# Performance work log

Measured on AMD Instinct MI355X. Metric: run time of the kernel, lower is better.

The kernel has to match this reference:

```python
import jax, jax.numpy as jnp
import numpy as np

N, C, D, K = 4096, 512, 64, 10  # samples, clusters (c_max), feature_dim, num_classes
KAPPA_N = 10.0


def setup_inputs() -> dict:
    key = jax.random.key(0)
    k1, k2, k3, k4, k5, k6 = jax.random.split(key, 6)
    data = jax.random.normal(k1, (N, D), dtype=jnp.float32)
    labels = jax.random.randint(k2, (N,), 0, K)
    # cluster support counts n >= kappa_n (mature clusters)
    n = jax.random.uniform(k3, (C,), dtype=jnp.float32) * 90.0 + KAPPA_N
    mu = jax.random.normal(k4, (C, D), dtype=jnp.float32) * 2.0
    # S is the scatter matrix; covariance Sigma = S / n must be SPD, so
    # build S = n * (0.1 * A A^T + 0.5 I)
    A = jax.random.normal(k5, (C, D, D), dtype=jnp.float32)
    AAT = jnp.einsum('cij,ckj->cik', A, A) / D
    S = n[:, None, None] * (0.1 * AAT + 0.5 * jnp.eye(D, dtype=jnp.float32))
    # one-hot class label per cluster
    cls = jax.random.randint(k6, (C,), 0, K)
    cluster_labels = jax.nn.one_hot(cls, K, dtype=jnp.int32)
    return {"data": data, "labels": labels, "n": n, "mu": mu, "S": S,
            "cluster_labels": cluster_labels}


def reference(data, labels, n, mu, S, cluster_labels):
    # Inference path of eGAUSSp.forward: for each sample z,
    #   Gamma_j = exp(-0.5 * (z - mu_j)^T (S_j / n_j)^{-1} (z - mu_j))   (all c clusters)
    #   scores  = defuzzify = sum_j Gamma_j * onehot(label_j) / sum_j Gamma_j
    # Vectorized over the batch (no cross-sample dependence in eval mode).
    eps = jnp.asarray(1e-6, data.dtype)
    Sigma = S / n[:, None, None] + eps * jnp.eye(S.shape[-1], dtype=data.dtype)  # [C,D,D]
    Sinv = jnp.linalg.inv(Sigma)                                                  # [C,D,D]
    diff = data[:, None, :] - mu[None, :, :]          # [N,C,D]
    tmp = jnp.einsum('ncd,cde->nce', diff, Sinv)      # [N,C,D]
    d2 = jnp.einsum('nce,nce->nc', tmp, diff)         # [N,C] squared Mahalanobis
    Gamma = jnp.exp(-0.5 * d2)                        # [N,C] activations
    lab_f = cluster_labels.astype(data.dtype)         # [C,K]
    scores = (Gamma @ lab_f) / (jnp.sum(Gamma, axis=1, keepdims=True) + 1e-12)  # [N,K]
    pred = jnp.argmax(scores, axis=1)
    clusters = jnp.argmax(Gamma, axis=1)
    return scores, pred, clusters
```

## Files before the change

### kernel.cpp

```cpp
#include <hip/hip_runtime.h>
#include <hip/hip_bf16.h>
#include <math.h>

#define NS 4096
#define NC 512
#define ND 64
#define NK 10
#define NPAIR 2080
#define KP 2176
#define BOFF 2080
#define KOFF 2144
#define KSPLIT 4
#define KT_PER (KP / 32 / KSPLIT)
#define ZB 1024
#define QB 2048

typedef __attribute__((ext_vector_type(8))) short short8;
typedef __attribute__((ext_vector_type(4))) float floatx4;

__device__ inline unsigned short f2b(float x) {
    __hip_bfloat16 h = __float2bfloat16(x);
    return __builtin_bit_cast(unsigned short, h);
}
__device__ inline float b2f(unsigned short u) {
    __hip_bfloat16 h = __builtin_bit_cast(__hip_bfloat16, u);
    return __bfloat162float(h);
}

__device__ inline float rlane(float v, int k) {
    return __builtin_bit_cast(float, __builtin_amdgcn_readlane(__builtin_bit_cast(int, v), k));
}

__device__ inline void gl16(const void* g, void* l) {
    __builtin_amdgcn_global_load_lds(
        (const __attribute__((address_space(1))) unsigned int*)g,
        (__attribute__((address_space(3))) unsigned int*)l, 16, 0, 0);
}

__device__ inline uchar2 ed_decode(int p) {
    if (p < NPAIR) {
        const float s = sqrtf((float)(16641 - 8 * p));
        int e = (int)((129.0f - s) * 0.5f);
        int off = e * 64 - (e * (e - 1)) / 2;
        const int offn = off + (64 - e);
        if (p >= offn) { off = offn; ++e; }
        else if (p < off) { off -= (65 - e); --e; }
        return make_uchar2((unsigned char)e, (unsigned char)(e + (p - off)));
    } else if (p < KOFF) return make_uchar2((unsigned char)(p - BOFF), 64);
    else if (p == KOFF)  return make_uchar2(64, 64);
    return make_uchar2(65, 65);
}

__global__ __launch_bounds__(256, 4) void prep_kernel(
    const float* __restrict__ data, const float* __restrict__ S,
    const float* __restrict__ n, const float* __restrict__ mu,
    const int* __restrict__ clab,
    unsigned short* __restrict__ Qh, unsigned short* __restrict__ Ql,
    unsigned short* __restrict__ Bph, unsigned short* __restrict__ Bpl,
    float* __restrict__ d2, float* __restrict__ labf)
{
    __shared__ float AcolS[ND * (ND + 1)];
    __shared__ float cbuf[ND];
    __shared__ float rowbuf[2][ND];
    __shared__ float kksS[1];
    __shared__ float zq[2][66];

    if (blockIdx.x >= NC + ZB) {
        const int qb = blockIdx.x - (NC + ZB);
        const int half = threadIdx.x >> 7;
        const int i = threadIdx.x & 127;
        const int row = qb * 2 + half;
        if (i < 64) zq[half][i] = data[(size_t)row * ND + i];
        else if (i == 64) { zq[half][64] = 1.0f; zq[half][65] = 0.0f; }
        __syncthreads();
        const float* __restrict__ zr = zq[half];
        unsigned short* __restrict__ qh = Qh + (size_t)row * KP;
        unsigned short* __restrict__ ql = Ql + (size_t)row * KP;
        #pragma unroll
        for (int t = 0; t < 17; ++t) {
            const int p = t * 128 + i;
            const uchar2 ed = ed_decode(p);
            const float v = zr[ed.x] * zr[ed.y];
            const unsigned short h = f2b(v);
            const unsigned short l = f2b(v - b2f(h));
            qh[p] = h;
            ql[p] = l;
        }
        return;
    }

    if (blockIdx.x >= NC) {
        const size_t base = (size_t)(blockIdx.x - NC) * 2048 + threadIdx.x * 8;
        *(float4*)&d2[base]     = make_float4(0.f, 0.f, 0.f, 0.f);
        *(float4*)&d2[base + 4] = make_float4(0.f, 0.f, 0.f, 0.f);
        return;
    }

    const int c = blockIdx.x;
    const int tid = threadIdx.x;
    const int j = tid & 63;
    const int w = tid >> 6;
    const int rbase = w * 16;

    const float inv_nc = 1.0f / n[c];
    const float* __restrict__ Sc = S + (size_t)c * ND * ND + j;

    float4 B0, B1, B2, B3;
#define LOADR(u) {                                                   \
    const float x0 = Sc[(rbase + 4*(u) + 0) * ND] * inv_nc;          \
    const float x1 = Sc[(rbase + 4*(u) + 1) * ND] * inv_nc;          \
    const float x2 = Sc[(rbase + 4*(u) + 2) * ND] * inv_nc;          \
    const float x3 = Sc[(rbase + 4*(u) + 3) * ND] * inv_nc;          \
    B##u.x = (rbase + 4*(u) + 0 == j) ? x0 + 1e-6f : x0;             \
    B##u.y = (rbase + 4*(u) + 1 == j) ? x1 + 1e-6f : x1;             \
    B##u.z = (rbase + 4*(u) + 2 == j) ? x2 + 1e-6f : x2;             \
    B##u.w = (rbase + 4*(u) + 3 == j) ? x3 + 1e-6f : x3; }
    LOADR(0) LOADR(1) LOADR(2) LOADR(3)
#undef LOADR

#define UPD4(u, K) {                                                  \
    const float c0 = rlane(B##u.x, K);                                \
    const float c1 = rlane(B##u.y, K);                                \
    const float c2 = rlane(B##u.z, K);                                \
    const float c3 = rlane(B##u.w, K);                                \
    B##u.x = (om && (4*(u)+0 == ((K)&15))) ? rowk : B##u.x * am - c0 * rowk; \
    B##u.y = (om && (4*(u)+1 == ((K)&15))) ? rowk : B##u.y * am - c1 * rowk; \
    B##u.z = (om && (4*(u)+2 == ((K)&15))) ? rowk : B##u.z * am - c2 * rowk; \
    B##u.w = (om && (4*(u)+3 == ((K)&15))) ? rowk : B##u.w * am - c3 * rowk; \
}
#define STEPC(TL, C, K) {                                             \
    if (w == ((K) >> 4)) {                                            \
        const float rp = B##TL.C;          \
        const float pv = rlane(rp, K);             \
        const float ip = 1.0f / pv;                                   \
        rowbuf[(K) & 1][j] = (j == (K)) ? ip : rp * ip;               \
    }                                                                 \
    __syncthreads();                                                  \
    const float rowk = rowbuf[(K) & 1][j];                            \
    const float am = (j == (K)) ? 0.0f : 1.0f;                        \
    const bool om = (w == ((K) >> 4));                                \
    UPD4(0, K) UPD4(1, K) UPD4(2, K) UPD4(3, K)                       \
}
#define STEP4(T, TL) STEPC(TL, x, 4*(T)+0) STEPC(TL, y, 4*(T)+1) \
                     STEPC(TL, z, 4*(T)+2) STEPC(TL, w, 4*(T)+3)
#define FOR16P(M) M(0,0) M(1,1) M(2,2) M(3,3) M(4,0) M(5,1) M(6,2) M(7,3) \
                  M(8,0) M(9,1) M(10,2) M(11,3) M(12,0) M(13,1) M(14,2) M(15,3)
    FOR16P(STEP4)
#undef FOR16P
#undef STEP4
#undef STEPC
#undef UPD4

#define MIR(u) *(float4*)&AcolS[j * (ND + 1) + rbase + 4*(u)] = B##u;
    MIR(0) MIR(1) MIR(2) MIR(3)
#undef MIR
    __syncthreads();

    if (w == 0) {
        const float* __restrict__ muc = mu + (size_t)c * ND;
        float y = 0.f;
        #pragma unroll
        for (int t = 0; t < 16; ++t) {
            const float4 v = *(const float4*)&AcolS[j * (ND + 1) + 4 * t];
            y += v.x * muc[4*t]     + v.y * muc[4*t + 1]
               + v.z * muc[4*t + 2] + v.w * muc[4*t + 3];
        }
        cbuf[j] = -2.0f * y;
        float kk = muc[j] * y;
        #pragma unroll
        for (int off = 32; off > 0; off >>= 1) kk += __shfl_down(kk, off);
        if (j == 0) {
            kksS[0] = kk;
            int lab = 0;
            for (int q = 0; q < NK; ++q) if (clab[c * NK + q] != 0) lab = q;
            labf[c] = (float)lab;
        }
    }
    __syncthreads();
    const float kks = kksS[0];

    unsigned short* __restrict__ ph = Bph + (size_t)c * KP;
    unsigned short* __restrict__ pl = Bpl + (size_t)c * KP;
    #pragma unroll
    for (int i = 0; i < 9; ++i) {
        const int t = w + 4 * i;
        if (t < KP / 64) {
            const int p = t * 64 + j;
            float val;
            if (p < NPAIR) {
                const uchar2 ed = ed_decode(p);
                val = (ed.x == ed.y) ? AcolS[ed.x * (ND + 1) + ed.x]
                    : (AcolS[ed.y * (ND + 1) + ed.x] + AcolS[ed.x * (ND + 1) + ed.y]);
            } else if (p < KOFF) val = cbuf[p - BOFF];
            else if (p == KOFF)  val = kks;
            else                 val = 0.f;
            const unsigned short h = f2b(val);
            const unsigned short l = f2b(val - b2f(h));
            ph[p] = h;
            pl[p] = l;
        }
    }
}

__global__ __launch_bounds__(256, 2) void gemm_kernel(
    const unsigned short* __restrict__ Qh, const unsigned short* __restrict__ Ql,
    const unsigned short* __restrict__ Bph, const unsigned short* __restrict__ Bpl,
    float* __restrict__ d2)
{
    __shared__ unsigned short AhS[2][64 * 32], AlS[2][64 * 32];
    __shared__ unsigned short BhS[2][256 * 32], BlS[2][256 * 32];

    const int tid  = threadIdx.x;
    const int lane = tid & 63, w = tid >> 6;
    const int quad = lane >> 4, rlo = lane & 15;

    const int lid = blockIdx.x + 64 * blockIdx.y + 128 * blockIdx.z;
    const int nyz = lid & 7;
    const int m0 = (lid >> 3) * 64;
    const int n0 = (nyz & 1) * 256;
    const int koff0 = (nyz >> 1) * KT_PER * 32;

    const int srow = tid >> 2;
    const int sswz = (tid & 3) ^ ((srow >> 2) & 3);
    const unsigned short* aGh = Qh + (size_t)(m0 + srow) * KP + koff0 + sswz * 8;
    const unsigned short* aGl = Ql + (size_t)(m0 + srow) * KP + koff0 + sswz * 8;
    const unsigned short* bGh[4];
    const unsigned short* bGl[4];
    #pragma unroll
    for (int rd = 0; rd < 4; ++rd) {
        const size_t off = (size_t)(n0 + rd * 64 + srow) * KP + koff0 + sswz * 8;
        bGh[rd] = Bph + off;
        bGl[rd] = Bpl + off;
    }
    const int swz8 = (quad ^ ((rlo >> 2) & 3)) * 8;

    floatx4 acc[4][4] = {};

#define STAGE(b, t) {                                                 \
        const int _ko = (t) * 32;                                     \
        gl16(aGh + _ko, &AhS[b][tid * 8]);                            \
        gl16(aGl + _ko, &AlS[b][tid * 8]);                            \
        _Pragma("unroll")                                             \
        for (int rd = 0; rd < 4; ++rd) {                              \
            gl16(bGh[rd] + _ko, &BhS[b][(rd * 256 + tid) * 8]);       \
            gl16(bGl[rd] + _ko, &BlS[b][(rd * 256 + tid) * 8]);       \
        } }

    STAGE(0, 0)
    STAGE(1, 1)
    asm volatile("s_waitcnt vmcnt(10)" ::: "memory");
    __builtin_amdgcn_s_barrier();

    for (int kt = 0; kt < KT_PER; ++kt) {
        const int cur = kt & 1;

        short8 ah[4], al[4], bh[4], bl[4];
        #pragma unroll
        for (int i = 0; i < 4; ++i) {
            ah[i] = *(const short8*)&AhS[cur][(i * 16 + rlo) * 32 + swz8];
            al[i] = *(const short8*)&AlS[cur][(i * 16 + rlo) * 32 + swz8];
        }
        #pragma unroll
        for (int j2 = 0; j2 < 4; ++j2) {
            const int r = w * 64 + j2 * 16 + rlo;
            bh[j2] = *(const short8*)&BhS[cur][r * 32 + swz8];
            bl[j2] = *(const short8*)&BlS[cur][r * 32 + swz8];
        }
        asm volatile("s_waitcnt lgkmcnt(0)" ::: "memory");
        __builtin_amdgcn_sched_barrier(0);
        __builtin_amdgcn_s_barrier();

        if (kt < KT_PER - 2) STAGE(cur, kt + 2)

        __builtin_amdgcn_s_setprio(1);
        #pragma unroll
        for (int i = 0; i < 4; ++i)
            #pragma unroll
            for (int j2 = 0; j2 < 4; ++j2) {
                acc[i][j2] = __builtin_amdgcn_mfma_f32_16x16x32_bf16(al[i], bh[j2], acc[i][j2], 0, 0, 0);
                acc[i][j2] = __builtin_amdgcn_mfma_f32_16x16x32_bf16(ah[i], bl[j2], acc[i][j2], 0, 0, 0);
                acc[i][j2] = __builtin_amdgcn_mfma_f32_16x16x32_bf16(ah[i], bh[j2], acc[i][j2], 0, 0, 0);
            }
        __builtin_amdgcn_s_setprio(0);

        if (kt < KT_PER - 2) {
            asm volatile("s_waitcnt vmcnt(10)" ::: "memory");
        } else {
            asm volatile("s_waitcnt vmcnt(0)" ::: "memory");
        }
        __builtin_amdgcn_s_barrier();
    }
#undef STAGE

    #pragma unroll
    for (int i = 0; i < 4; ++i)
        #pragma unroll
        for (int j2 = 0; j2 < 4; ++j2) {
            const int m = m0 + i * 16 + quad * 4;
            const int nn = n0 + w * 64 + j2 * 16 + rlo;
            #pragma unroll
            for (int r = 0; r < 4; ++r)
                atomicAdd(&d2[(size_t)(m + r) * NC + nn], acc[i][j2][r]);
        }
}

__global__ __launch_bounds__(256) void score_kernel(
    const float* __restrict__ d2, const float* __restrict__ labf,
    float* __restrict__ out)
{
    const int s = blockIdx.x * 4 + (threadIdx.x >> 6);
    const int l = threadIdx.x & 63;

    float numer[NK];
    #pragma unroll
    for (int q = 0; q < NK; ++q) numer[q] = 0.f;
    float denom = 0.f, gmax = -1.f;
    int gidx = 0;

    #pragma unroll
    for (int i = 0; i < NC / 256; ++i) {
        const int c0 = i * 256 + l * 4;
        const float4 v = *(const float4*)&d2[(size_t)s * NC + c0];
        #pragma unroll
        for (int r = 0; r < 4; ++r) {
            const int c = c0 + r;
            const float G = __expf(-0.5f * ((const float*)&v)[r]);
            denom += G;
            const int lab = (int)labf[c];
            #pragma unroll
            for (int q = 0; q < NK; ++q) numer[q] += (q == lab) ? G : 0.f;
            if (G > gmax) { gmax = G; gidx = c; }
        }
    }

    #pragma unroll
    for (int off = 32; off > 0; off >>= 1) {
        const float og = __shfl_down(gmax, off);
        const int   oi = __shfl_down(gidx, off);
        if (og > gmax || (og == gmax && oi < gidx)) { gmax = og; gidx = oi; }
        denom += __shfl_down(denom, off);
        #pragma unroll
        for (int q = 0; q < NK; ++q) numer[q] += __shfl_down(numer[q], off);
    }

    if (l == 0) {
        const float inv = 1.0f / (denom + 1e-12f);
        float best = -1.f; int pk = 0;
        #pragma unroll
        for (int q = 0; q < NK; ++q) {
            const float sc = numer[q] * inv;
            out[(size_t)s * NK + q] = sc;
            if (sc > best) { best = sc; pk = q; }
        }
        out[(size_t)NS * NK + s]      = (float)pk;
        out[(size_t)NS * NK + NS + s] = (float)gidx;
    }
}

extern "C" void kernel_launch(void* const* d_in, const int* in_sizes, int n_in,
                              void* d_out, int out_size, void* d_ws, size_t ws_size,
                              hipStream_t stream)
{
    const float* data = (const float*)d_in[0];
    const float* n    = (const float*)d_in[2];
    const float* mu   = (const float*)d_in[3];
    const float* S    = (const float*)d_in[4];
    const int*   clab = (const int*)d_in[5];

    char* w = (char*)d_ws;
    unsigned short* Qh  = (unsigned short*)(w);
    unsigned short* Ql  = (unsigned short*)(w + 17825792);
    unsigned short* Bph = (unsigned short*)(w + 35651584);
    unsigned short* Bpl = (unsigned short*)(w + 37879808);
    float* d2   = (float*)(w + 40108032);
    float* labf = (float*)(w + 48496640);

    hipLaunchKernelGGL(prep_kernel,  dim3(NC + ZB + QB), dim3(256), 0, stream,
                       data, S, n, mu, clab, Qh, Ql, Bph, Bpl, d2, labf);
    hipLaunchKernelGGL(gemm_kernel,  dim3(NS / 64, NC / 256, KSPLIT), dim3(256), 0, stream,
                       Qh, Ql, Bph, Bpl, d2);
    hipLaunchKernelGGL(score_kernel, dim3(NS / 4), dim3(256), 0, stream,
                       d2, labf, (float*)d_out);
}
```

Baseline: 149.2 us.

## Fuse prep, GEMM and scoring into one cooperative kernel with grid syncs

Replaces the three separate launches (prep, split-K GEMM, score) with a single cooperative kernel of 512 blocks. Each block zeroes part of d2, builds Q rows for 8 samples and inverts one cluster covariance, then passes a grid sync, runs one GEMM tile, passes another grid sync and scores 8 samples. This removes launch gaps and kernel boundaries, at the cost of grid-wide barriers. It also needs every block resident at once under the shared-memory union and launch bounds, and the prep phase runs on fewer blocks than before.

```diff
diff --git a/kernel.cpp b/kernel.cpp
--- a/kernel.cpp
+++ b/kernel.cpp
@@ -1,6 +1,9 @@
 #include <hip/hip_runtime.h>
+#include <hip/hip_cooperative_groups.h>
 #include <hip/hip_bf16.h>
 #include <math.h>
+
+namespace cg = cooperative_groups;
 
 #define NS 4096
 #define NC 512
@@ -12,8 +15,6 @@
 #define KOFF 2144
 #define KSPLIT 4
 #define KT_PER (KP / 32 / KSPLIT)
-#define ZB 1024
-#define QB 2048
 
 typedef __attribute__((ext_vector_type(8))) short short8;
 typedef __attribute__((ext_vector_type(4))) float floatx4;
@@ -51,61 +52,81 @@
     return make_uchar2(65, 65);
 }
 
-__global__ __launch_bounds__(256, 4) void prep_kernel(
+union SmemU {
+    struct {
+        unsigned short AhS[2][64 * 32], AlS[2][64 * 32];
+        unsigned short BhS[2][256 * 32], BlS[2][256 * 32];
+    } g;
+    struct {
+        float AcolS[ND * (ND + 1)];
+        float cbuf[ND];
+        float rowbuf[2][ND];
+        float kks[1];
+        float zq[8][66];
+    } p;
+};
+
+__global__ __launch_bounds__(256, 2) void mega_kernel(
     const float* __restrict__ data, const float* __restrict__ S,
     const float* __restrict__ n, const float* __restrict__ mu,
     const int* __restrict__ clab,
     unsigned short* __restrict__ Qh, unsigned short* __restrict__ Ql,
     unsigned short* __restrict__ Bph, unsigned short* __restrict__ Bpl,
-    float* __restrict__ d2, float* __restrict__ labf)
+    float* __restrict__ d2, float* __restrict__ labf, float* __restrict__ out)
 {
-    __shared__ float AcolS[ND * (ND + 1)];
-    __shared__ float cbuf[ND];
-    __shared__ float rowbuf[2][ND];
-    __shared__ float kksS[1];
-    __shared__ float zq[2][66];
-
-    if (blockIdx.x >= NC + ZB) {
-        const int qb = blockIdx.x - (NC + ZB);
-        const int half = threadIdx.x >> 7;
-        const int i = threadIdx.x & 127;
-        const int row = qb * 2 + half;
-        if (i < 64) zq[half][i] = data[(size_t)row * ND + i];
-        else if (i == 64) { zq[half][64] = 1.0f; zq[half][65] = 0.0f; }
+    __shared__ SmemU sm;
+    cg::grid_group grid = cg::this_grid();
+
+    const int tid  = threadIdx.x;
+    const int lane = tid & 63, w = tid >> 6;
+    const int quad = lane >> 4, rlo = lane & 15;
+    const int blk  = blockIdx.x;
+
+    {
+        const size_t base = (size_t)blk * 4096 + tid * 16;
+        *(float4*)&d2[base]      = make_float4(0.f, 0.f, 0.f, 0.f);
+        *(float4*)&d2[base + 4]  = make_float4(0.f, 0.f, 0.f, 0.f);
+        *(float4*)&d2[base + 8]  = make_float4(0.f, 0.f, 0.f, 0.f);
+        *(float4*)&d2[base + 12] = make_float4(0.f, 0.f, 0.f, 0.f);
+    }
+
+    {
+        const int r8 = tid >> 5;
+        const int cc = (tid & 31) * 2;
+        sm.p.zq[r8][cc]     = data[(size_t)(blk * 8 + r8) * ND + cc];
+        sm.p.zq[r8][cc + 1] = data[(size_t)(blk * 8 + r8) * ND + cc + 1];
+        if ((tid & 31) == 0) { sm.p.zq[r8][64] = 1.0f; sm.p.zq[r8][65] = 0.0f; }
         __syncthreads();
-        const float* __restrict__ zr = zq[half];
-        unsigned short* __restrict__ qh = Qh + (size_t)row * KP;
-        unsigned short* __restrict__ ql = Ql + (size_t)row * KP;
-        #pragma unroll
-        for (int t = 0; t < 17; ++t) {
-            const int p = t * 128 + i;
-            const uchar2 ed = ed_decode(p);
-            const float v = zr[ed.x] * zr[ed.y];
-            const unsigned short h = f2b(v);
-            const unsigned short l = f2b(v - b2f(h));
-            qh[p] = h;
-            ql[p] = l;
-        }
-        return;
-    }
-
-    if (blockIdx.x >= NC) {
-        const size_t base = (size_t)(blockIdx.x - NC) * 2048 + threadIdx.x * 8;
-        *(float4*)&d2[base]     = make_float4(0.f, 0.f, 0.f, 0.f);
-        *(float4*)&d2[base + 4] = make_float4(0.f, 0.f, 0.f, 0.f);
-        return;
-    }
-
-    const int c = blockIdx.x;
-    const int tid = threadIdx.x;
-    const int j = tid & 63;
-    const int w = tid >> 6;
-    const int rbase = w * 16;
-
-    const float inv_nc = 1.0f / n[c];
-    const float* __restrict__ Sc = S + (size_t)c * ND * ND + j;
-
-    float4 B0, B1, B2, B3;
+        const int half = tid >> 7;
+        const int i = tid & 127;
+        #pragma unroll
+        for (int rr = 0; rr < 4; ++rr) {
+            const int row = blk * 8 + rr * 2 + half;
+            const float* __restrict__ zr = sm.p.zq[rr * 2 + half];
+            unsigned short* __restrict__ qh = Qh + (size_t)row * KP;
+            unsigned short* __restrict__ ql = Ql + (size_t)row * KP;
+            #pragma unroll
+            for (int t = 0; t < 17; ++t) {
+                const int p = t * 128 + i;
+                const uchar2 ed = ed_decode(p);
+                const float v = zr[ed.x] * zr[ed.y];
+                const unsigned short h = f2b(v);
+                const unsigned short l = f2b(v - b2f(h));
+                qh[p] = h;
+                ql[p] = l;
+            }
+        }
+    }
+
+    {
+        const int c = blk;
+        const int j = lane;
+        const int rbase = w * 16;
+
+        const float inv_nc = 1.0f / n[c];
+        const float* __restrict__ Sc = S + (size_t)c * ND * ND + j;
+
+        float4 B0, B1, B2, B3;
 #define LOADR(u) {                                                   \
     const float x0 = Sc[(rbase + 4*(u) + 0) * ND] * inv_nc;          \
     const float x1 = Sc[(rbase + 4*(u) + 1) * ND] * inv_nc;          \
@@ -115,7 +136,7 @@
     B##u.y = (rbase + 4*(u) + 1 == j) ? x1 + 1e-6f : x1;             \
     B##u.z = (rbase + 4*(u) + 2 == j) ? x2 + 1e-6f : x2;             \
     B##u.w = (rbase + 4*(u) + 3 == j) ? x3 + 1e-6f : x3; }
-    LOADR(0) LOADR(1) LOADR(2) LOADR(3)
+        LOADR(0) LOADR(1) LOADR(2) LOADR(3)
 #undef LOADR
 
 #define UPD4(u, K) {                                                  \
@@ -130,13 +151,13 @@
 }
 #define STEPC(TL, C, K) {                                             \
     if (w == ((K) >> 4)) {                                            \
-        const float rp = B##TL.C;          \
-        const float pv = rlane(rp, K);             \
+        const float rp = B##TL.C;                                     \
+        const float pv = rlane(rp, K);                                \
         const float ip = 1.0f / pv;                                   \
-        rowbuf[(K) & 1][j] = (j == (K)) ? ip : rp * ip;               \
+        sm.p.rowbuf[(K) & 1][j] = (j == (K)) ? ip : rp * ip;          \
     }                                                                 \
     __syncthreads();                                                  \
-    const float rowk = rowbuf[(K) & 1][j];                            \
+    const float rowk = sm.p.rowbuf[(K) & 1][j];                       \
     const float am = (j == (K)) ? 0.0f : 1.0f;                        \
     const bool om = (w == ((K) >> 4));                                \
     UPD4(0, K) UPD4(1, K) UPD4(2, K) UPD4(3, K)                       \
@@ -145,215 +166,209 @@
                      STEPC(TL, z, 4*(T)+2) STEPC(TL, w, 4*(T)+3)
 #define FOR16P(M) M(0,0) M(1,1) M(2,2) M(3,3) M(4,0) M(5,1) M(6,2) M(7,3) \
                   M(8,0) M(9,1) M(10,2) M(11,3) M(12,0) M(13,1) M(14,2) M(15,3)
-    FOR16P(STEP4)
+        FOR16P(STEP4)
 #undef FOR16P
 #undef STEP4
 #undef STEPC
 #undef UPD4
 
-#define MIR(u) *(float4*)&AcolS[j * (ND + 1) + rbase + 4*(u)] = B##u;
-    MIR(0) MIR(1) MIR(2) MIR(3)
+#define MIR(u) *(float4*)&sm.p.AcolS[j * (ND + 1) + rbase + 4*(u)] = B##u;
+        MIR(0) MIR(1) MIR(2) MIR(3)
 #undef MIR
-    __syncthreads();
-
-    if (w == 0) {
-        const float* __restrict__ muc = mu + (size_t)c * ND;
-        float y = 0.f;
-        #pragma unroll
-        for (int t = 0; t < 16; ++t) {
-            const float4 v = *(const float4*)&AcolS[j * (ND + 1) + 4 * t];
-            y += v.x * muc[4*t]     + v.y * muc[4*t + 1]
-               + v.z * muc[4*t + 2] + v.w * muc[4*t + 3];
-        }
-        cbuf[j] = -2.0f * y;
-        float kk = muc[j] * y;
-        #pragma unroll
-        for (int off = 32; off > 0; off >>= 1) kk += __shfl_down(kk, off);
-        if (j == 0) {
-            kksS[0] = kk;
-            int lab = 0;
-            for (int q = 0; q < NK; ++q) if (clab[c * NK + q] != 0) lab = q;
-            labf[c] = (float)lab;
-        }
-    }
-    __syncthreads();
-    const float kks = kksS[0];
-
-    unsigned short* __restrict__ ph = Bph + (size_t)c * KP;
-    unsigned short* __restrict__ pl = Bpl + (size_t)c * KP;
-    #pragma unroll
-    for (int i = 0; i < 9; ++i) {
-        const int t = w + 4 * i;
-        if (t < KP / 64) {
-            const int p = t * 64 + j;
-            float val;
-            if (p < NPAIR) {
-                const uchar2 ed = ed_decode(p);
-                val = (ed.x == ed.y) ? AcolS[ed.x * (ND + 1) + ed.x]
-                    : (AcolS[ed.y * (ND + 1) + ed.x] + AcolS[ed.x * (ND + 1) + ed.y]);
-            } else if (p < KOFF) val = cbuf[p - BOFF];
-            else if (p == KOFF)  val = kks;
-            else                 val = 0.f;
-            const unsigned short h = f2b(val);
-            const unsigned short l = f2b(val - b2f(h));
-            ph[p] = h;
-            pl[p] = l;
-        }
-    }
-}
-
-__global__ __launch_bounds__(256, 2) void gemm_kernel(
-    const unsigned short* __restrict__ Qh, const unsigned short* __restrict__ Ql,
-    const unsigned short* __restrict__ Bph, const unsigned short* __restrict__ Bpl,
-    float* __restrict__ d2)
-{
-    __shared__ unsigned short AhS[2][64 * 32], AlS[2][64 * 32];
-    __shared__ unsigned short BhS[2][256 * 32], BlS[2][256 * 32];
-
-    const int tid  = threadIdx.x;
-    const int lane = tid & 63, w = tid >> 6;
-    const int quad = lane >> 4, rlo = lane & 15;
-
-    const int lid = blockIdx.x + 64 * blockIdx.y + 128 * blockIdx.z;
-    const int nyz = lid & 7;
-    const int m0 = (lid >> 3) * 64;
-    const int n0 = (nyz & 1) * 256;
-    const int koff0 = (nyz >> 1) * KT_PER * 32;
-
-    const int srow = tid >> 2;
-    const int sswz = (tid & 3) ^ ((srow >> 2) & 3);
-    const unsigned short* aGh = Qh + (size_t)(m0 + srow) * KP + koff0 + sswz * 8;
-    const unsigned short* aGl = Ql + (size_t)(m0 + srow) * KP + koff0 + sswz * 8;
-    const unsigned short* bGh[4];
-    const unsigned short* bGl[4];
-    #pragma unroll
-    for (int rd = 0; rd < 4; ++rd) {
-        const size_t off = (size_t)(n0 + rd * 64 + srow) * KP + koff0 + sswz * 8;
-        bGh[rd] = Bph + off;
-        bGl[rd] = Bpl + off;
-    }
-    const int swz8 = (quad ^ ((rlo >> 2) & 3)) * 8;
-
-    floatx4 acc[4][4] = {};
+        __syncthreads();
+
+        if (w == 0) {
+            const float* __restrict__ muc = mu + (size_t)c * ND;
+            float y = 0.f;
+            #pragma unroll
+            for (int t = 0; t < 16; ++t) {
+                const float4 v = *(const float4*)&sm.p.AcolS[j * (ND + 1) + 4 * t];
+                y += v.x * muc[4*t]     + v.y * muc[4*t + 1]
+                   + v.z * muc[4*t + 2] + v.w * muc[4*t + 3];
+            }
+            sm.p.cbuf[j] = -2.0f * y;
+            float kk = muc[j] * y;
+            #pragma unroll
+            for (int off = 32; off > 0; off >>= 1) kk += __shfl_down(kk, off);
+            if (j == 0) {
+                sm.p.kks[0] = kk;
+                int lab = 0;
+                for (int q = 0; q < NK; ++q) if (clab[c * NK + q] != 0) lab = q;
+                labf[c] = (float)lab;
+            }
+        }
+        __syncthreads();
+        const float kks = sm.p.kks[0];
+
+        unsigned short* __restrict__ ph = Bph + (size_t)c * KP;
+        unsigned short* __restrict__ pl = Bpl + (size_t)c * KP;
+        #pragma unroll
+        for (int i2 = 0; i2 < 9; ++i2) {
+            const int t = w + 4 * i2;
+            if (t < KP / 64) {
+                const int p = t * 64 + j;
+                float val;
+                if (p < NPAIR) {
+                    const uchar2 ed = ed_decode(p);
+                    val = (ed.x == ed.y) ? sm.p.AcolS[ed.x * (ND + 1) + ed.x]
+                        : (sm.p.AcolS[ed.y * (ND + 1) + ed.x] + sm.p.AcolS[ed.x * (ND + 1) + ed.y]);
+                } else if (p < KOFF) val = sm.p.cbuf[p - BOFF];
+                else if (p == KOFF)  val = kks;
+                else                 val = 0.f;
+                const unsigned short h = f2b(val);
+                const unsigned short l = f2b(val - b2f(h));
+                ph[p] = h;
+                pl[p] = l;
+            }
+        }
+    }
+
+    grid.sync();
+
+    {
+        const int lid = blk;
+        const int nyz = lid & 7;
+        const int m0 = (lid >> 3) * 64;
+        const int n0 = (nyz & 1) * 256;
+        const int koff0 = (nyz >> 1) * KT_PER * 32;
+
+        const int srow = tid >> 2;
+        const int sswz = (tid & 3) ^ ((srow >> 2) & 3);
+        const unsigned short* aGh = Qh + (size_t)(m0 + srow) * KP + koff0 + sswz * 8;
+        const unsigned short* aGl = Ql + (size_t)(m0 + srow) * KP + koff0 + sswz * 8;
+        const unsigned short* bGh[4];
+        const unsigned short* bGl[4];
+        #pragma unroll
+        for (int rd = 0; rd < 4; ++rd) {
+            const size_t off = (size_t)(n0 + rd * 64 + srow) * KP + koff0 + sswz * 8;
+            bGh[rd] = Bph + off;
+            bGl[rd] = Bpl + off;
+        }
+        const int swz8 = (quad ^ ((rlo >> 2) & 3)) * 8;
+
+        floatx4 acc[4][4] = {};
 
 #define STAGE(b, t) {                                                 \
         const int _ko = (t) * 32;                                     \
-        gl16(aGh + _ko, &AhS[b][tid * 8]);                            \
-        gl16(aGl + _ko, &AlS[b][tid * 8]);                            \
+        gl16(aGh + _ko, &sm.g.AhS[b][tid * 8]);                       \
+        gl16(aGl + _ko, &sm.g.AlS[b][tid * 8]);                       \
         _Pragma("unroll")                                             \
         for (int rd = 0; rd < 4; ++rd) {                              \
-            gl16(bGh[rd] + _ko, &BhS[b][(rd * 256 + tid) * 8]);       \
-            gl16(bGl[rd] + _ko, &BlS[b][(rd * 256 + tid) * 8]);       \
+            gl16(bGh[rd] + _ko, &sm.g.BhS[b][(rd * 256 + tid) * 8]);  \
+            gl16(bGl[rd] + _ko, &sm.g.BlS[b][(rd * 256 + tid) * 8]);  \
         } }
 
-    STAGE(0, 0)
-    STAGE(1, 1)
-    asm volatile("s_waitcnt vmcnt(10)" ::: "memory");
-    __builtin_amdgcn_s_barrier();
-
-    for (int kt = 0; kt < KT_PER; ++kt) {
-        const int cur = kt & 1;
-
-        short8 ah[4], al[4], bh[4], bl[4];
-        #pragma unroll
-        for (int i = 0; i < 4; ++i) {
-            ah[i] = *(const short8*)&AhS[cur][(i * 16 + rlo) * 32 + swz8];
-            al[i] = *(const short8*)&AlS[cur][(i * 16 + rlo) * 32 + swz8];
-        }
-        #pragma unroll
-        for (int j2 = 0; j2 < 4; ++j2) {
-            const int r = w * 64 + j2 * 16 + rlo;
-            bh[j2] = *(const short8*)&BhS[cur][r * 32 + swz8];
-            bl[j2] = *(const short8*)&BlS[cur][r * 32 + swz8];
-        }
-        asm volatile("s_waitcnt lgkmcnt(0)" ::: "memory");
-        __builtin_amdgcn_sched_barrier(0);
+        STAGE(0, 0)
+        STAGE(1, 1)
+        asm volatile("s_waitcnt vmcnt(10)" ::: "memory");
         __builtin_amdgcn_s_barrier();
 
-        if (kt < KT_PER - 2) STAGE(cur, kt + 2)
-
-        __builtin_amdgcn_s_setprio(1);
+        for (int kt = 0; kt < KT_PER; ++kt) {
+            const int cur = kt & 1;
+
+            short8 ah[4], al[4], bh[4], bl[4];
+            #pragma unroll
+            for (int i = 0; i < 4; ++i) {
+                ah[i] = *(const short8*)&sm.g.AhS[cur][(i * 16 + rlo) * 32 + swz8];
+                al[i] = *(const short8*)&sm.g.AlS[cur][(i * 16 + rlo) * 32 + swz8];
+            }
+            #pragma unroll
+            for (int j2 = 0; j2 < 4; ++j2) {
+                const int r = w * 64 + j2 * 16 + rlo;
+                bh[j2] = *(const short8*)&sm.g.BhS[cur][r * 32 + swz8];
+                bl[j2] = *(const short8*)&sm.g.BlS[cur][r * 32 + swz8];
+            }
+            asm volatile("s_waitcnt lgkmcnt(0)" ::: "memory");
+            __builtin_amdgcn_sched_barrier(0);
+            __builtin_amdgcn_s_barrier();
+
+            if (kt < KT_PER - 2) STAGE(cur, kt + 2)
+
+            __builtin_amdgcn_s_setprio(1);
+            #pragma unroll
+            for (int i = 0; i < 4; ++i)
+                #pragma unroll
+                for (int j2 = 0; j2 < 4; ++j2) {
+                    acc[i][j2] = __builtin_amdgcn_mfma_f32_16x16x32_bf16(al[i], bh[j2], acc[i][j2], 0, 0, 0);
+                    acc[i][j2] = __builtin_amdgcn_mfma_f32_16x16x32_bf16(ah[i], bl[j2], acc[i][j2], 0, 0, 0);
+                    acc[i][j2] = __builtin_amdgcn_mfma_f32_16x16x32_bf16(ah[i], bh[j2], acc[i][j2], 0, 0, 0);
+                }
+            __builtin_amdgcn_s_setprio(0);
+
+            if (kt < KT_PER - 2) {
+                asm volatile("s_waitcnt vmcnt(10)" ::: "memory");
+            } else {
+                asm volatile("s_waitcnt vmcnt(0)" ::: "memory");
+            }
+            __builtin_amdgcn_s_barrier();
+        }
+#undef STAGE
+
         #pragma unroll
         for (int i = 0; i < 4; ++i)
             #pragma unroll
             for (int j2 = 0; j2 < 4; ++j2) {
-                acc[i][j2] = __builtin_amdgcn_mfma_f32_16x16x32_bf16(al[i], bh[j2], acc[i][j2], 0, 0, 0);
-                acc[i][j2] = __builtin_amdgcn_mfma_f32_16x16x32_bf16(ah[i], bl[j2], acc[i][j2], 0, 0, 0);
-                acc[i][j2] = __builtin_amdgcn_mfma_f32_16x16x32_bf16(ah[i], bh[j2], acc[i][j2], 0, 0, 0);
-            }
-        __builtin_amdgcn_s_setprio(0);
-
-        if (kt < KT_PER - 2) {
-            asm volatile("s_waitcnt vmcnt(10)" ::: "memory");
-        } else {
-            asm volatile("s_waitcnt vmcnt(0)" ::: "memory");
-        }
-        __builtin_amdgcn_s_barrier();
-    }
-#undef STAGE
-
-    #pragma unroll
-    for (int i = 0; i < 4; ++i)
-        #pragma unroll
-        for (int j2 = 0; j2 < 4; ++j2) {
-            const int m = m0 + i * 16 + quad * 4;
-            const int nn = n0 + w * 64 + j2 * 16 + rlo;
-            #pragma unroll
-            for (int r = 0; r < 4; ++r)
-                atomicAdd(&d2[(size_t)(m + r) * NC + nn], acc[i][j2][r]);
-        }
-}
-
-__global__ __launch_bounds__(256) void score_kernel(
-    const float* __restrict__ d2, const float* __restrict__ labf,
-    float* __restrict__ out)
-{
-    const int s = blockIdx.x * 4 + (threadIdx.x >> 6);
-    const int l = threadIdx.x & 63;
-
-    float numer[NK];
-    #pragma unroll
-    for (int q = 0; q < NK; ++q) numer[q] = 0.f;
-    float denom = 0.f, gmax = -1.f;
-    int gidx = 0;
-
-    #pragma unroll
-    for (int i = 0; i < NC / 256; ++i) {
-        const int c0 = i * 256 + l * 4;
-        const float4 v = *(const float4*)&d2[(size_t)s * NC + c0];
-        #pragma unroll
-        for (int r = 0; r < 4; ++r) {
-            const int c = c0 + r;
-            const float G = __expf(-0.5f * ((const float*)&v)[r]);
-            denom += G;
-            const int lab = (int)labf[c];
-            #pragma unroll
-            for (int q = 0; q < NK; ++q) numer[q] += (q == lab) ? G : 0.f;
-            if (G > gmax) { gmax = G; gidx = c; }
-        }
-    }
-
-    #pragma unroll
-    for (int off = 32; off > 0; off >>= 1) {
-        const float og = __shfl_down(gmax, off);
-        const int   oi = __shfl_down(gidx, off);
-        if (og > gmax || (og == gmax && oi < gidx)) { gmax = og; gidx = oi; }
-        denom += __shfl_down(denom, off);
-        #pragma unroll
-        for (int q = 0; q < NK; ++q) numer[q] += __shfl_down(numer[q], off);
-    }
-
-    if (l == 0) {
-        const float inv = 1.0f / (denom + 1e-12f);
-        float best = -1.f; int pk = 0;
-        #pragma unroll
-        for (int q = 0; q < NK; ++q) {
-            const float sc = numer[q] * inv;
-            out[(size_t)s * NK + q] = sc;
-            if (sc > best) { best = sc; pk = q; }
-        }
-        out[(size_t)NS * NK + s]      = (float)pk;
-        out[(size_t)NS * NK + NS + s] = (float)gidx;
+                const int m = m0 + i * 16 + quad * 4;
+                const int nn = n0 + w * 64 + j2 * 16 + rlo;
+                #pragma unroll
+                for (int r = 0; r < 4; ++r)
+                    atomicAdd(&d2[(size_t)(m + r) * NC + nn], acc[i][j2][r]);
+            }
+    }
+
+    grid.sync();
+
+    {
+        const int l = lane;
+        #pragma unroll
+        for (int it = 0; it < 2; ++it) {
+            const int s = blk * 8 + w * 2 + it;
+
+            float numer[NK];
+            #pragma unroll
+            for (int q = 0; q < NK; ++q) numer[q] = 0.f;
+            float denom = 0.f, gmax = -1.f;
+            int gidx = 0;
+
+            #pragma unroll
+            for (int i = 0; i < NC / 256; ++i) {
+                const int c0 = i * 256 + l * 4;
+                const float4 v = *(const float4*)&d2[(size_t)s * NC + c0];
+                #pragma unroll
+                for (int r = 0; r < 4; ++r) {
+                    const int c = c0 + r;
+                    const float G = __expf(-0.5f * ((const float*)&v)[r]);
+                    denom += G;
+                    const int lab = (int)labf[c];
+                    #pragma unroll
+                    for (int q = 0; q < NK; ++q) numer[q] += (q == lab) ? G : 0.f;
+                    if (G > gmax) { gmax = G; gidx = c; }
+                }
+            }
+
+            #pragma unroll
+            for (int off = 32; off > 0; off >>= 1) {
+                const float og = __shfl_down(gmax, off);
+                const int   oi = __shfl_down(gidx, off);
+                if (og > gmax || (og == gmax && oi < gidx)) { gmax = og; gidx = oi; }
+                denom += __shfl_down(denom, off);
+                #pragma unroll
+                for (int q = 0; q < NK; ++q) numer[q] += __shfl_down(numer[q], off);
+            }
+
+            if (l == 0) {
+                const float inv = 1.0f / (denom + 1e-12f);
+                float best = -1.f; int pk = 0;
+                #pragma unroll
+                for (int q = 0; q < NK; ++q) {
+                    const float sc = numer[q] * inv;
+                    out[(size_t)s * NK + q] = sc;
+                    if (sc > best) { best = sc; pk = q; }
+                }
+                out[(size_t)NS * NK + s]      = (float)pk;
+                out[(size_t)NS * NK + NS + s] = (float)gidx;
+            }
+        }
     }
 }
 
@@ -374,11 +389,11 @@
     unsigned short* Bpl = (unsigned short*)(w + 37879808);
     float* d2   = (float*)(w + 40108032);
     float* labf = (float*)(w + 48496640);
-
-    hipLaunchKernelGGL(prep_kernel,  dim3(NC + ZB + QB), dim3(256), 0, stream,
-                       data, S, n, mu, clab, Qh, Ql, Bph, Bpl, d2, labf);
-    hipLaunchKernelGGL(gemm_kernel,  dim3(NS / 64, NC / 256, KSPLIT), dim3(256), 0, stream,
-                       Qh, Ql, Bph, Bpl, d2);
-    hipLaunchKernelGGL(score_kernel, dim3(NS / 4), dim3(256), 0, stream,
-                       d2, labf, (float*)d_out);
-}
+    float* out  = (float*)d_out;
+
+    void* args[] = { (void*)&data, (void*)&S, (void*)&n, (void*)&mu,
+                     (void*)&clab, (void*)&Qh, (void*)&Ql, (void*)&Bph,
+                     (void*)&Bpl, (void*)&d2, (void*)&labf, (void*)&out };
+    hipLaunchCooperativeKernel((const void*)mega_kernel, dim3(NC), dim3(256),
+                               args, 0, stream);
+}
```

Measured after the change: 285.7 us. 91.5% more time.
